# Kernel optimization log

Hardware: AMD Instinct MI355X
Metric: run time of the kernel (lower is better)

## Reference

```python
import jax, jax.numpy as jnp
import numpy as np
import math

N_HEAD = 16
HEAD_DIM = 64
N_EMBD = 1024
EPS_RMS = 1e-5
U_L2_EPS = 1e-6

def _get_alibi_slopes(n_heads):
    def pow2(n):
        start = 2 ** (-2 ** (-(math.log2(n) - 3)))
        return [start * start ** i for i in range(n)]
    if math.log2(n_heads).is_integer():
        return pow2(n_heads)
    c = 2 ** math.floor(math.log2(n_heads))
    s = pow2(c)
    extra = _get_alibi_slopes(2 * c)
    return s + extra[0::2][: n_heads - c]

def setup_inputs() -> dict:
    key = jax.random.key(0)
    ks = jax.random.split(key, 9)
    B, T = 2, 2048
    H, D, C = N_HEAD, HEAD_DIM, N_EMBD
    x = jax.random.normal(ks[0], (B, T, C), dtype=jnp.float32)
    # Linear weights stored as [in, out] so y = x @ W
    sc = 1.0 / math.sqrt(C)
    Wq = jax.random.normal(ks[1], (C, H * D), dtype=jnp.float32) * sc
    Wk = jax.random.normal(ks[2], (C, H * D), dtype=jnp.float32) * sc
    Wv = jax.random.normal(ks[3], (C, H * D), dtype=jnp.float32) * sc
    Wproj = jax.random.normal(ks[4], (H * D, C), dtype=jnp.float32) * (0.5 / math.sqrt(C) / math.sqrt(12))
    q_rms_w = jnp.ones((D,), dtype=jnp.float32)
    k_rms_w = jnp.ones((D,), dtype=jnp.float32)
    # keygated bias params: omega init = softplus_inverse(1.0), u ~ N(0, 1/sqrt(D))
    omega = jnp.full((H,), math.log(math.expm1(1.0)), dtype=jnp.float32)
    u = jax.random.normal(ks[5], (H, D), dtype=jnp.float32) * (1.0 / math.sqrt(D))
    return {"x": x, "Wq": Wq, "Wk": Wk, "Wv": Wv, "Wproj": Wproj,
            "q_rms_w": q_rms_w, "k_rms_w": k_rms_w, "omega": omega, "u": u}

def _rmsnorm(x, w):
    var = jnp.mean(jnp.square(x), axis=-1, keepdims=True)
    return x * jax.lax.rsqrt(var + EPS_RMS) * w

def reference(x, Wq, Wk, Wv, Wproj, q_rms_w, k_rms_w, omega, u):
    B, T, C = x.shape
    H, D = N_HEAD, HEAD_DIM
    q = (x @ Wq).reshape(B, T, H, D)
    k = (x @ Wk).reshape(B, T, H, D)
    v = (x @ Wv).reshape(B, T, H, D)
    q = _rmsnorm(q, q_rms_w)
    k = _rmsnorm(k, k_rms_w)
    # key-gated additive bias
    slopes = jnp.asarray(_get_alibi_slopes(H), dtype=jnp.float32)  # [H]
    omega_eff = jax.nn.softplus(omega) * slopes                    # [H]
    u_n = u / jnp.maximum(jnp.linalg.norm(u, axis=-1, keepdims=True), U_L2_EPS)
    gate_logits = jnp.einsum('bthd,hd->bht', k, u_n) / math.sqrt(D)  # fp32
    gate = jax.nn.softplus(gate_logits)                            # [B,H,T]
    idx = jnp.arange(T)
    dist = jnp.maximum(idx[:, None] - idx[None, :], 0).astype(jnp.float32)  # [T,T]
    bias = -dist[None, None] * omega_eff[None, :, None, None] * gate[:, :, None, :]  # [B,H,T,T]
    causal = idx[:, None] >= idx[None, :]
    bias = jnp.where(causal[None, None], bias, -jnp.inf)
    # attention
    scale = 1.0 / math.sqrt(D)
    scores = jnp.einsum('bihd,bjhd->bhij', q, k) * scale + bias
    attn = jax.nn.softmax(scores, axis=-1)
    y = jnp.einsum('bhij,bjhd->bihd', attn, v).reshape(B, T, H * D)
    return y @ Wproj
```

## Files before the change

### kernel.cpp

```cpp
#include <hip/hip_runtime.h>
#include <hip/hip_bf16.h>

#define NH 16
#define HD 64
#define CE 1024
#define TT 2048
#define BB 2
#define MR (BB*TT)
#define SWZ(r) ((((r) & 7)) ^ (((r) >> 3) & 3))

typedef __attribute__((ext_vector_type(4))) float f32x4;
typedef __attribute__((ext_vector_type(16))) float f32x16;
typedef __attribute__((ext_vector_type(8))) short s16x8;
typedef unsigned int u32;
typedef unsigned short u16;

__device__ __forceinline__ void gld16(const void* g, void* l) {
  __builtin_amdgcn_global_load_lds((const __attribute__((address_space(1))) unsigned int*)g,
                                   (__attribute__((address_space(3))) unsigned int*)l, 16, 0, 0);
}
__device__ __forceinline__ u16 f2b(float f) {
  union { __hip_bfloat16 b; u16 u; } t;
  t.b = __float2bfloat16(f);
  return t.u;
}
__device__ __forceinline__ u32 pk2(float a, float b) {
  return (u32)f2b(a) | ((u32)f2b(b) << 16);
}
__device__ __forceinline__ float red64_sum(float v) {
#pragma unroll
  for (int m = 1; m < 64; m <<= 1) v += __shfl_xor(v, m, 64);
  return v;
}
__device__ __forceinline__ float softplusf(float x) {
  return x > 20.0f ? x : log1pf(expf(x));
}

__global__ __launch_bounds__(256) void cvt_x(const float* __restrict__ x,
                                             u16* __restrict__ xb, int n4) {
  int stride = gridDim.x * blockDim.x;
  for (int i = blockIdx.x * blockDim.x + threadIdx.x; i < n4; i += stride) {
    float4 v = ((const float4*)x)[i];
    union { u16 u[4]; uint2 p; } o;
    o.u[0] = f2b(v.x); o.u[1] = f2b(v.y); o.u[2] = f2b(v.z); o.u[3] = f2b(v.w);
    ((uint2*)xb)[i] = o.p;
  }
}

__global__ __launch_bounds__(256) void cvt_wt(const float* __restrict__ W0, const float* __restrict__ W1,
                                              const float* __restrict__ W2, const float* __restrict__ W3,
                                              u16* __restrict__ T0, u16* __restrict__ T1,
                                              u16* __restrict__ T2, u16* __restrict__ T3) {
  const float* W = blockIdx.z == 0 ? W0 : blockIdx.z == 1 ? W1 : blockIdx.z == 2 ? W2 : W3;
  u16* T = blockIdx.z == 0 ? T0 : blockIdx.z == 1 ? T1 : blockIdx.z == 2 ? T2 : T3;
  __shared__ float t[64][65];
  int k0 = blockIdx.x * 64, n0 = blockIdx.y * 64;
  int row = threadIdx.x >> 2, seg = threadIdx.x & 3;
#pragma unroll
  for (int i = 0; i < 4; ++i) {
    float4 v = *(const float4*)(W + (size_t)(k0 + row) * CE + n0 + seg * 16 + i * 4);
    int c = seg * 16 + i * 4;
    t[row][c + 0] = v.x; t[row][c + 1] = v.y; t[row][c + 2] = v.z; t[row][c + 3] = v.w;
  }
  __syncthreads();
#pragma unroll
  for (int it = 0; it < 2; ++it) {
    int c = threadIdx.x + it * 256;
    int n = c >> 3, ks = (c & 7) * 8;
    union { u16 u[8]; uint4 p; } o;
#pragma unroll
    for (int e = 0; e < 8; ++e) o.u[e] = f2b(t[ks + e][n]);
    *(uint4*)(T + (size_t)(n0 + n) * CE + k0 + ks) = o.p;
  }
}

#define BM 128
#define BN 128
#define BK 64
__global__ __launch_bounds__(256) void gemm3(const u16* __restrict__ A,
    const u16* __restrict__ B0, const u16* __restrict__ B1,
    const u16* __restrict__ B2,
    float* __restrict__ C0, float* __restrict__ C1, float* __restrict__ C2,
    int M, int N, int K) {
  const u16* Bt = blockIdx.z == 0 ? B0 : blockIdx.z == 1 ? B1 : B2;
  float* C = blockIdx.z == 0 ? C0 : blockIdx.z == 1 ? C1 : C2;
  __shared__ __align__(16) u16 aT[BM * BK];
  __shared__ __align__(16) u16 bT[BN * BK];
  int tid = threadIdx.x;
  int w = tid >> 6, lane = tid & 63, q4 = lane >> 4, r16 = lane & 15;
  int m0 = blockIdx.y * BM, n0 = blockIdx.x * BN;
  int wm = (w >> 1) * 64, wn = (w & 1) * 64;
  f32x4 acc[4][4] = {};
  for (int k0 = 0; k0 < K; k0 += BK) {
#pragma unroll
    for (int it = 0; it < 4; ++it) {
      int c = tid + it * 256;
      int row = c >> 3, sl = c & 7;
      gld16(A + (size_t)(m0 + row) * K + k0 + ((sl ^ SWZ(row)) << 3), &aT[c * 8]);
      gld16(Bt + (size_t)(n0 + row) * K + k0 + ((sl ^ SWZ(row)) << 3), &bT[c * 8]);
    }
    __syncthreads();
#pragma unroll
    for (int kk = 0; kk < 2; ++kk) {
      s16x8 af[4], bfr[4];
#pragma unroll
      for (int i = 0; i < 4; ++i) {
        int ra = wm + i * 16 + r16;
        af[i] = *(const s16x8*)((char*)aT + ra * 128 + ((((kk << 2) | q4) ^ SWZ(ra)) << 4));
        int rb = wn + i * 16 + r16;
        bfr[i] = *(const s16x8*)((char*)bT + rb * 128 + ((((kk << 2) | q4) ^ SWZ(rb)) << 4));
      }
#pragma unroll
      for (int i = 0; i < 4; ++i)
#pragma unroll
        for (int j = 0; j < 4; ++j)
          acc[i][j] = __builtin_amdgcn_mfma_f32_16x16x32_bf16(af[i], bfr[j], acc[i][j], 0, 0, 0);
    }
    __syncthreads();
  }
#pragma unroll
  for (int i = 0; i < 4; ++i)
#pragma unroll
    for (int j = 0; j < 4; ++j)
#pragma unroll
      for (int r = 0; r < 4; ++r) {
        int gm = m0 + wm + i * 16 + (q4 << 2) + r;
        int gn = n0 + wn + j * 16 + r16;
        C[(size_t)gm * N + gn] = acc[i][j][r];
      }
}

__global__ __launch_bounds__(256) void rmsgate(const float* __restrict__ q, const float* __restrict__ k,
    const float* __restrict__ v, const float* __restrict__ qw, const float* __restrict__ kw,
    const float* __restrict__ omega, const float* __restrict__ u,
    u16* __restrict__ qb, u16* __restrict__ kb,
    u16* __restrict__ vtb, float* __restrict__ cg) {
  int b = blockIdx.z, h = blockIdx.y, t0 = blockIdx.x * 64;
  int tid = threadIdx.x, w = tid >> 6, lane = tid & 63;
  float uv = u[h * HD + lane];
  float us = red64_sum(uv * uv);
  float un = uv / fmaxf(sqrtf(us), 1e-6f);
  float qwl = qw[lane], kwl = kw[lane];
  float weff = softplusf(omega[h]) * exp2f(-0.5f * (float)(h + 1));
  size_t hb = ((size_t)(b * NH + h)) * TT;
#pragma unroll 4
  for (int it = 0; it < 16; ++it) {
    int t = t0 + w * 16 + it;
    size_t roff = ((size_t)(b * TT + t)) * CE + h * HD + lane;
    float qv = q[roff];
    float rq = rsqrtf(red64_sum(qv * qv) * (1.0f / 64.0f) + 1e-5f);
    qb[(hb + t) * HD + lane] = f2b(qv * rq * qwl * 0.125f);
    float kv = k[roff];
    float rk = rsqrtf(red64_sum(kv * kv) * (1.0f / 64.0f) + 1e-5f);
    float kn = kv * rk * kwl;
    kb[(hb + t) * HD + lane] = f2b(kn);
    float gl = red64_sum(kn * un) * 0.125f;
    if (lane == 0) cg[hb + t] = weff * softplusf(gl);
  }
  __shared__ u16 vt[64 * 65];
  int row = tid >> 2, seg = tid & 3;
#pragma unroll
  for (int i = 0; i < 4; ++i) {
    float4 vv = *(const float4*)(v + ((size_t)(b * TT + t0 + row)) * CE + h * HD + seg * 16 + i * 4);
    int d = seg * 16 + i * 4;
    vt[(d + 0) * 65 + row] = f2b(vv.x);
    vt[(d + 1) * 65 + row] = f2b(vv.y);
    vt[(d + 2) * 65 + row] = f2b(vv.z);
    vt[(d + 3) * 65 + row] = f2b(vv.w);
  }
  __syncthreads();
#pragma unroll
  for (int it = 0; it < 2; ++it) {
    int c = tid + it * 256;
    int d = c >> 3, js = (c & 7) * 8;
    union { u16 u[8]; uint4 p; } o;
#pragma unroll
    for (int e = 0; e < 8; ++e) o.u[e] = vt[d * 65 + js + e];
    *(uint4*)(vtb + (((size_t)(b * NH + h)) * HD + d) * TT + t0 + js) = o.p;
  }
}

#define KVB 64
__global__ __launch_bounds__(256) void attn(const u16* __restrict__ qb,
    const u16* __restrict__ kb, const u16* __restrict__ vtb,
    const float* __restrict__ cg, u16* __restrict__ y) {
  int b = blockIdx.z, h = blockIdx.y, qb0 = blockIdx.x * 128;
  int tid = threadIdx.x, w = tid >> 6, lane = tid & 63;
  int hi = lane >> 5, q5 = lane & 31;
  __shared__ __align__(16) u16 kl[64 * 64];
  __shared__ __align__(16) u16 vl[64 * 64];
  __shared__ float cgl[KVB];
  size_t hb = ((size_t)(b * NH + h)) * TT;
  size_t vbase = ((size_t)(b * NH + h)) * HD;
  int qrow = qb0 + w * 32 + q5;
  s16x8 qf[4];
#pragma unroll
  for (int kc = 0; kc < 4; ++kc)
    qf[kc] = *(const s16x8*)(qb + (hb + qrow) * HD + kc * 16 + hi * 8);
  f32x16 accO[2] = {};
  float m = -1e30f, l = 0.f;
  int qhi = qb0 + w * 32 + 31;
  int nt = (qb0 + 128) / KVB;
  for (int jt = 0; jt < nt; ++jt) {
    int j0 = jt * KVB;
#pragma unroll
    for (int it = 0; it < 2; ++it) {
      int c = tid + (it << 8);
      int row = c >> 3, sl = c & 7;
      gld16(kb + (hb + j0 + row) * HD + ((sl ^ SWZ(row)) << 3), &kl[c * 8]);
      gld16(vtb + (vbase + row) * TT + j0 + ((sl ^ SWZ(row)) << 3), &vl[c * 8]);
    }
    if (tid < KVB) cgl[tid] = cg[hb + j0 + tid];
    __syncthreads();
    if (j0 <= qhi) {
      f32x16 s0 = {}, s1 = {};
#pragma unroll
      for (int kc = 0; kc < 4; ++kc) {
        int r0 = q5;
        s16x8 kf0 = *(const s16x8*)((char*)kl + r0 * 128 + ((((kc << 1) | hi) ^ SWZ(r0)) << 4));
        s0 = __builtin_amdgcn_mfma_f32_32x32x16_bf16(kf0, qf[kc], s0, 0, 0, 0);
        int r1 = q5 + 32;
        s16x8 kf1 = *(const s16x8*)((char*)kl + r1 * 128 + ((((kc << 1) | hi) ^ SWZ(r1)) << 4));
        s1 = __builtin_amdgcn_mfma_f32_32x32x16_bf16(kf1, qf[kc], s1, 0, 0, 0);
      }
      float pmax = -1e30f;
#pragma unroll
      for (int r = 0; r < 16; ++r) {
        int kvl = (r & 3) + 8 * (r >> 2) + 4 * hi;
        int j = j0 + kvl;
        float sv = s0[r];
        sv = (j <= qrow) ? sv - (float)(qrow - j) * cgl[kvl] : -1e30f;
        s0[r] = sv; pmax = fmaxf(pmax, sv);
        int j2 = j0 + 32 + kvl;
        float sv1 = s1[r];
        sv1 = (j2 <= qrow) ? sv1 - (float)(qrow - j2) * cgl[32 + kvl] : -1e30f;
        s1[r] = sv1; pmax = fmaxf(pmax, sv1);
      }
      pmax = fmaxf(pmax, __shfl_xor(pmax, 32, 64));
      float mn = fmaxf(m, pmax);
      float al = __expf(m - mn);
      m = mn;
      float ps = 0.f;
#pragma unroll
      for (int r = 0; r < 16; ++r) {
        float p0 = __expf(s0[r] - m); s0[r] = p0;
        float p1 = __expf(s1[r] - m); s1[r] = p1;
        ps += p0 + p1;
      }
      ps += __shfl_xor(ps, 32, 64);
      l = l * al + ps;
#pragma unroll
      for (int r = 0; r < 16; ++r) { accO[0][r] *= al; accO[1][r] *= al; }
      auto pvchunk = [&](f32x16 sc, int cb4) {
        u32 c01 = pk2(sc[0], sc[1]),  c23 = pk2(sc[2], sc[3]);
        u32 c45 = pk2(sc[4], sc[5]),  c67 = pk2(sc[6], sc[7]);
        u32 c89 = pk2(sc[8], sc[9]),  cAB = pk2(sc[10], sc[11]);
        u32 cCD = pk2(sc[12], sc[13]), cEF = pk2(sc[14], sc[15]);
        u32 x01 = (u32)__shfl_xor((int)c01, 32, 64), x23 = (u32)__shfl_xor((int)c23, 32, 64);
        u32 x45 = (u32)__shfl_xor((int)c45, 32, 64), x67 = (u32)__shfl_xor((int)c67, 32, 64);
        u32 x89 = (u32)__shfl_xor((int)c89, 32, 64), xAB = (u32)__shfl_xor((int)cAB, 32, 64);
        u32 xCD = (u32)__shfl_xor((int)cCD, 32, 64), xEF = (u32)__shfl_xor((int)cEF, 32, 64);
        union { u32 wd[4]; s16x8 v; } Bf0, Bf1;
        Bf0.wd[0] = hi ? x45 : c01; Bf0.wd[1] = hi ? x67 : c23;
        Bf0.wd[2] = hi ? c45 : x01; Bf0.wd[3] = hi ? c67 : x23;
        Bf1.wd[0] = hi ? xCD : c89; Bf1.wd[1] = hi ? xEF : cAB;
        Bf1.wd[2] = hi ? cCD : x89; Bf1.wd[3] = hi ? cEF : xAB;
#pragma unroll
        for (int dt = 0; dt < 2; ++dt) {
          int dr = q5 + 32 * dt;
          s16x8 vf0 = *(const s16x8*)((char*)vl + dr * 128 + (((cb4 | hi) ^ SWZ(dr)) << 4));
          s16x8 vf1 = *(const s16x8*)((char*)vl + dr * 128 + ((((cb4 | 2) | hi) ^ SWZ(dr)) << 4));
          accO[dt] = __builtin_amdgcn_mfma_f32_32x32x16_bf16(vf0, Bf0.v, accO[dt], 0, 0, 0);
          accO[dt] = __builtin_amdgcn_mfma_f32_32x32x16_bf16(vf1, Bf1.v, accO[dt], 0, 0, 0);
        }
      };
      pvchunk(s0, 0);
      pvchunk(s1, 4);
    }
    __syncthreads();
  }
  u16* obase = (w < 2) ? (kl + w * 2048) : (vl + (w - 2) * 2048);
  float inv = 1.f / l;
#pragma unroll
  for (int dt = 0; dt < 2; ++dt)
#pragma unroll
    for (int r = 0; r < 16; ++r) {
      int d = 32 * dt + (r & 3) + 8 * (r >> 2) + 4 * hi;
      *(u16*)((char*)obase + q5 * 128 + ((((d >> 3)) ^ SWZ(q5)) << 4) + ((d & 7) << 1)) = f2b(accO[dt][r] * inv);
    }
  __syncthreads();
  int row = lane >> 1, half = lane & 1;
#pragma unroll
  for (int s4 = 0; s4 < 4; ++s4) {
    int slot = half * 4 + s4;
    s16x8 vv = *(const s16x8*)((char*)obase + row * 128 + ((slot ^ SWZ(row)) << 4));
    *(s16x8*)(y + ((size_t)(b * TT) + qb0 + w * 32 + row) * CE + h * HD + half * 32 + s4 * 8) = vv;
  }
}

extern "C" void kernel_launch(void* const* d_in, const int* in_sizes, int n_in,
                              void* d_out, int out_size, void* d_ws, size_t ws_size,
                              hipStream_t stream) {
  const float* x  = (const float*)d_in[0];
  const float* Wq = (const float*)d_in[1];
  const float* Wk = (const float*)d_in[2];
  const float* Wv = (const float*)d_in[3];
  const float* Wp = (const float*)d_in[4];
  const float* qw = (const float*)d_in[5];
  const float* kw = (const float*)d_in[6];
  const float* om = (const float*)d_in[7];
  const float* u  = (const float*)d_in[8];
  float* out = (float*)d_out;
  char* ws = (char*)d_ws;
  const size_t MB = 1024 * 1024;
  u16* xb  = (u16*)(ws + 0);
  u16* wqt = (u16*)(ws + 8 * MB);
  u16* wkt = (u16*)(ws + 10 * MB);
  u16* wvt = (u16*)(ws + 12 * MB);
  u16* wpt = (u16*)(ws + 14 * MB);
  float* qf = (float*)(ws + 16 * MB);
  float* kf = (float*)(ws + 32 * MB);
  float* vf = (float*)(ws + 48 * MB);
  u16* qbb = (u16*)(ws + 64 * MB);
  u16* kbb = (u16*)(ws + 72 * MB);
  u16* vtb = (u16*)(ws + 80 * MB);
  float* cg = (float*)(ws + 88 * MB);
  u16* yb = (u16*)(ws + 16 * MB);

  cvt_x<<<dim3(2048), dim3(256), 0, stream>>>(x, xb, MR * CE / 4);
  cvt_wt<<<dim3(16, 16, 4), dim3(256), 0, stream>>>(Wq, Wk, Wv, Wp, wqt, wkt, wvt, wpt);
  gemm3<<<dim3(8, 32, 3), dim3(256), 0, stream>>>(xb, wqt, wkt, wvt, qf, kf, vf, MR, CE, CE);
  rmsgate<<<dim3(32, 16, 2), dim3(256), 0, stream>>>(qf, kf, vf, qw, kw, om, u, qbb, kbb, vtb, cg);
  attn<<<dim3(16, 16, 2), dim3(256), 0, stream>>>(qbb, kbb, vtb, cg, yb);
  gemm3<<<dim3(8, 32, 1), dim3(256), 0, stream>>>(yb, wpt, wpt, wpt, out, out, out, MR, CE, CE);
}
```

Before: 307.3 us.

## Restructure attention into single-wave blocks loading K/V straight to registers

Result: slower. 325.7 us (+6.0%).

```diff
diff --git a/kernel.cpp b/kernel.cpp
--- a/kernel.cpp
+++ b/kernel.cpp
@@ -8,6 +8,7 @@
 #define BB 2
 #define MR (BB*TT)
 #define SWZ(r) ((((r) & 7)) ^ (((r) >> 3) & 3))
+#define LOG2E 1.44269504f
 
 typedef __attribute__((ext_vector_type(4))) float f32x4;
 typedef __attribute__((ext_vector_type(16))) float f32x16;
@@ -141,7 +142,7 @@
   float us = red64_sum(uv * uv);
   float un = uv / fmaxf(sqrtf(us), 1e-6f);
   float qwl = qw[lane], kwl = kw[lane];
-  float weff = softplusf(omega[h]) * exp2f(-0.5f * (float)(h + 1));
+  float weff = softplusf(omega[h]) * exp2f(-0.5f * (float)(h + 1)) * LOG2E;
   size_t hb = ((size_t)(b * NH + h)) * TT;
 #pragma unroll 4
   for (int it = 0; it < 16; ++it) {
@@ -149,7 +150,7 @@
     size_t roff = ((size_t)(b * TT + t)) * CE + h * HD + lane;
     float qv = q[roff];
     float rq = rsqrtf(red64_sum(qv * qv) * (1.0f / 64.0f) + 1e-5f);
-    qb[(hb + t) * HD + lane] = f2b(qv * rq * qwl * 0.125f);
+    qb[(hb + t) * HD + lane] = f2b(qv * rq * qwl * (0.125f * LOG2E));
     float kv = k[roff];
     float rk = rsqrtf(red64_sum(kv * kv) * (1.0f / 64.0f) + 1e-5f);
     float kn = kv * rk * kwl;
@@ -181,120 +182,131 @@
 }
 
 #define KVB 64
-__global__ __launch_bounds__(256) void attn(const u16* __restrict__ qb,
+__global__ __launch_bounds__(64) void attn(const u16* __restrict__ qb,
     const u16* __restrict__ kb, const u16* __restrict__ vtb,
     const float* __restrict__ cg, u16* __restrict__ y) {
-  int b = blockIdx.z, h = blockIdx.y, qb0 = blockIdx.x * 128;
-  int tid = threadIdx.x, w = tid >> 6, lane = tid & 63;
+  int b = blockIdx.z, h = blockIdx.y;
+  int qt = gridDim.x - 1 - blockIdx.x;
+  int lane = threadIdx.x & 63;
   int hi = lane >> 5, q5 = lane & 31;
-  __shared__ __align__(16) u16 kl[64 * 64];
-  __shared__ __align__(16) u16 vl[64 * 64];
-  __shared__ float cgl[KVB];
+  __shared__ __align__(16) u16 ol[32 * 64];
   size_t hb = ((size_t)(b * NH + h)) * TT;
   size_t vbase = ((size_t)(b * NH + h)) * HD;
-  int qrow = qb0 + w * 32 + q5;
+  int qrow = qt * 32 + q5;
+  const u16* qptr = qb + (hb + qrow) * HD;
   s16x8 qf[4];
 #pragma unroll
   for (int kc = 0; kc < 4; ++kc)
-    qf[kc] = *(const s16x8*)(qb + (hb + qrow) * HD + kc * 16 + hi * 8);
+    qf[kc] = *(const s16x8*)(qptr + kc * 16 + hi * 8);
   f32x16 accO[2] = {};
   float m = -1e30f, l = 0.f;
-  int qhi = qb0 + w * 32 + 31;
-  int nt = (qb0 + 128) / KVB;
+  int nt = qt / 2 + 1;
   for (int jt = 0; jt < nt; ++jt) {
     int j0 = jt * KVB;
-#pragma unroll
-    for (int it = 0; it < 2; ++it) {
-      int c = tid + (it << 8);
-      int row = c >> 3, sl = c & 7;
-      gld16(kb + (hb + j0 + row) * HD + ((sl ^ SWZ(row)) << 3), &kl[c * 8]);
-      gld16(vtb + (vbase + row) * TT + j0 + ((sl ^ SWZ(row)) << 3), &vl[c * 8]);
-    }
-    if (tid < KVB) cgl[tid] = cg[hb + j0 + tid];
-    __syncthreads();
-    if (j0 <= qhi) {
-      f32x16 s0 = {}, s1 = {};
-#pragma unroll
-      for (int kc = 0; kc < 4; ++kc) {
-        int r0 = q5;
-        s16x8 kf0 = *(const s16x8*)((char*)kl + r0 * 128 + ((((kc << 1) | hi) ^ SWZ(r0)) << 4));
-        s0 = __builtin_amdgcn_mfma_f32_32x32x16_bf16(kf0, qf[kc], s0, 0, 0, 0);
-        int r1 = q5 + 32;
-        s16x8 kf1 = *(const s16x8*)((char*)kl + r1 * 128 + ((((kc << 1) | hi) ^ SWZ(r1)) << 4));
-        s1 = __builtin_amdgcn_mfma_f32_32x32x16_bf16(kf1, qf[kc], s1, 0, 0, 0);
-      }
-      float pmax = -1e30f;
-#pragma unroll
-      for (int r = 0; r < 16; ++r) {
-        int kvl = (r & 3) + 8 * (r >> 2) + 4 * hi;
-        int j = j0 + kvl;
-        float sv = s0[r];
-        sv = (j <= qrow) ? sv - (float)(qrow - j) * cgl[kvl] : -1e30f;
-        s0[r] = sv; pmax = fmaxf(pmax, sv);
-        int j2 = j0 + 32 + kvl;
-        float sv1 = s1[r];
-        sv1 = (j2 <= qrow) ? sv1 - (float)(qrow - j2) * cgl[32 + kvl] : -1e30f;
-        s1[r] = sv1; pmax = fmaxf(pmax, sv1);
-      }
-      pmax = fmaxf(pmax, __shfl_xor(pmax, 32, 64));
-      float mn = fmaxf(m, pmax);
-      float al = __expf(m - mn);
-      m = mn;
-      float ps = 0.f;
-#pragma unroll
-      for (int r = 0; r < 16; ++r) {
-        float p0 = __expf(s0[r] - m); s0[r] = p0;
-        float p1 = __expf(s1[r] - m); s1[r] = p1;
-        ps += p0 + p1;
-      }
-      ps += __shfl_xor(ps, 32, 64);
-      l = l * al + ps;
-#pragma unroll
-      for (int r = 0; r < 16; ++r) { accO[0][r] *= al; accO[1][r] *= al; }
-      auto pvchunk = [&](f32x16 sc, int cb4) {
-        u32 c01 = pk2(sc[0], sc[1]),  c23 = pk2(sc[2], sc[3]);
-        u32 c45 = pk2(sc[4], sc[5]),  c67 = pk2(sc[6], sc[7]);
-        u32 c89 = pk2(sc[8], sc[9]),  cAB = pk2(sc[10], sc[11]);
-        u32 cCD = pk2(sc[12], sc[13]), cEF = pk2(sc[14], sc[15]);
-        u32 x01 = (u32)__shfl_xor((int)c01, 32, 64), x23 = (u32)__shfl_xor((int)c23, 32, 64);
-        u32 x45 = (u32)__shfl_xor((int)c45, 32, 64), x67 = (u32)__shfl_xor((int)c67, 32, 64);
-        u32 x89 = (u32)__shfl_xor((int)c89, 32, 64), xAB = (u32)__shfl_xor((int)cAB, 32, 64);
-        u32 xCD = (u32)__shfl_xor((int)cCD, 32, 64), xEF = (u32)__shfl_xor((int)cEF, 32, 64);
-        union { u32 wd[4]; s16x8 v; } Bf0, Bf1;
-        Bf0.wd[0] = hi ? x45 : c01; Bf0.wd[1] = hi ? x67 : c23;
-        Bf0.wd[2] = hi ? c45 : x01; Bf0.wd[3] = hi ? c67 : x23;
-        Bf1.wd[0] = hi ? xCD : c89; Bf1.wd[1] = hi ? xEF : cAB;
-        Bf1.wd[2] = hi ? cCD : x89; Bf1.wd[3] = hi ? cEF : xAB;
-#pragma unroll
-        for (int dt = 0; dt < 2; ++dt) {
-          int dr = q5 + 32 * dt;
-          s16x8 vf0 = *(const s16x8*)((char*)vl + dr * 128 + (((cb4 | hi) ^ SWZ(dr)) << 4));
-          s16x8 vf1 = *(const s16x8*)((char*)vl + dr * 128 + ((((cb4 | 2) | hi) ^ SWZ(dr)) << 4));
-          accO[dt] = __builtin_amdgcn_mfma_f32_32x32x16_bf16(vf0, Bf0.v, accO[dt], 0, 0, 0);
-          accO[dt] = __builtin_amdgcn_mfma_f32_32x32x16_bf16(vf1, Bf1.v, accO[dt], 0, 0, 0);
-        }
-      };
-      pvchunk(s0, 0);
-      pvchunk(s1, 4);
-    }
-    __syncthreads();
-  }
-  u16* obase = (w < 2) ? (kl + w * 2048) : (vl + (w - 2) * 2048);
+    const u16* kp0 = kb + (hb + j0 + q5) * HD + hi * 8;
+    const u16* kp1 = kb + (hb + j0 + 32 + q5) * HD + hi * 8;
+    s16x8 kf0[4], kf1[4];
+#pragma unroll
+    for (int kc = 0; kc < 4; ++kc) {
+      kf0[kc] = *(const s16x8*)(kp0 + kc * 16);
+      kf1[kc] = *(const s16x8*)(kp1 + kc * 16);
+    }
+    const u16* vp0 = vtb + (vbase + q5) * TT + j0 + hi * 8;
+    const u16* vp1 = vtb + (vbase + 32 + q5) * TT + j0 + hi * 8;
+    s16x8 vfr0[4], vfr1[4];
+#pragma unroll
+    for (int c = 0; c < 4; ++c) {
+      vfr0[c] = *(const s16x8*)(vp0 + c * 16);
+      vfr1[c] = *(const s16x8*)(vp1 + c * 16);
+    }
+    const float* cgp = cg + hb + j0 + 4 * hi;
+    f32x4 cgA[4], cgB[4];
+#pragma unroll
+    for (int g = 0; g < 4; ++g) {
+      cgA[g] = *(const f32x4*)(cgp + 8 * g);
+      cgB[g] = *(const f32x4*)(cgp + 32 + 8 * g);
+    }
+    f32x16 s0 = {}, s1 = {};
+#pragma unroll
+    for (int kc = 0; kc < 4; ++kc) {
+      s0 = __builtin_amdgcn_mfma_f32_32x32x16_bf16(kf0[kc], qf[kc], s0, 0, 0, 0);
+      s1 = __builtin_amdgcn_mfma_f32_32x32x16_bf16(kf1[kc], qf[kc], s1, 0, 0, 0);
+    }
+    float dif0 = (float)(qrow - j0);
+#pragma unroll
+    for (int r = 0; r < 16; ++r) {
+      float kvlf = (float)((r & 3) + 8 * (r >> 2) + 4 * hi);
+      float d0 = dif0 - kvlf;
+      float d1 = d0 - 32.f;
+      float cg0 = cgA[r >> 2][r & 3], cg1 = cgB[r >> 2][r & 3];
+      s0[r] = (d0 >= 0.f) ? s0[r] - d0 * cg0 : -1e30f;
+      s1[r] = (d1 >= 0.f) ? s1[r] - d1 * cg1 : -1e30f;
+    }
+    float t8[8];
+#pragma unroll
+    for (int i = 0; i < 8; ++i)
+      t8[i] = fmaxf(fmaxf(s0[i], s0[i + 8]), fmaxf(s1[i], s1[i + 8]));
+    float t4a = fmaxf(t8[0], t8[4]), t4b = fmaxf(t8[1], t8[5]);
+    float t4c = fmaxf(t8[2], t8[6]), t4d = fmaxf(t8[3], t8[7]);
+    float pmax = fmaxf(fmaxf(t4a, t4b), fmaxf(t4c, t4d));
+    pmax = fmaxf(pmax, __shfl_xor(pmax, 32, 64));
+    float mn = fmaxf(m, pmax);
+    float al = exp2f(m - mn);
+    m = mn;
+#pragma unroll
+    for (int r = 0; r < 16; ++r) {
+      s0[r] = exp2f(s0[r] - m);
+      s1[r] = exp2f(s1[r] - m);
+    }
+    float e8[8];
+#pragma unroll
+    for (int i = 0; i < 8; ++i)
+      e8[i] = (s0[i] + s0[i + 8]) + (s1[i] + s1[i + 8]);
+    float e4a = e8[0] + e8[4], e4b = e8[1] + e8[5];
+    float e4c = e8[2] + e8[6], e4d = e8[3] + e8[7];
+    float ps = (e4a + e4b) + (e4c + e4d);
+    ps += __shfl_xor(ps, 32, 64);
+    l = l * al + ps;
+#pragma unroll
+    for (int r = 0; r < 16; ++r) { accO[0][r] *= al; accO[1][r] *= al; }
+    auto pvchunk = [&](const f32x16& sc, const s16x8& v00, const s16x8& v01,
+                       const s16x8& v10, const s16x8& v11) {
+      u32 c01 = pk2(sc[0], sc[1]),  c23 = pk2(sc[2], sc[3]);
+      u32 c45 = pk2(sc[4], sc[5]),  c67 = pk2(sc[6], sc[7]);
+      u32 c89 = pk2(sc[8], sc[9]),  cAB = pk2(sc[10], sc[11]);
+      u32 cCD = pk2(sc[12], sc[13]), cEF = pk2(sc[14], sc[15]);
+      u32 x01 = (u32)__shfl_xor((int)c01, 32, 64), x23 = (u32)__shfl_xor((int)c23, 32, 64);
+      u32 x45 = (u32)__shfl_xor((int)c45, 32, 64), x67 = (u32)__shfl_xor((int)c67, 32, 64);
+      u32 x89 = (u32)__shfl_xor((int)c89, 32, 64), xAB = (u32)__shfl_xor((int)cAB, 32, 64);
+      u32 xCD = (u32)__shfl_xor((int)cCD, 32, 64), xEF = (u32)__shfl_xor((int)cEF, 32, 64);
+      union { u32 wd[4]; s16x8 v; } Bf0, Bf1;
+      Bf0.wd[0] = hi ? x45 : c01; Bf0.wd[1] = hi ? x67 : c23;
+      Bf0.wd[2] = hi ? c45 : x01; Bf0.wd[3] = hi ? c67 : x23;
+      Bf1.wd[0] = hi ? xCD : c89; Bf1.wd[1] = hi ? xEF : cAB;
+      Bf1.wd[2] = hi ? cCD : x89; Bf1.wd[3] = hi ? cEF : xAB;
+      accO[0] = __builtin_amdgcn_mfma_f32_32x32x16_bf16(v00, Bf0.v, accO[0], 0, 0, 0);
+      accO[0] = __builtin_amdgcn_mfma_f32_32x32x16_bf16(v01, Bf1.v, accO[0], 0, 0, 0);
+      accO[1] = __builtin_amdgcn_mfma_f32_32x32x16_bf16(v10, Bf0.v, accO[1], 0, 0, 0);
+      accO[1] = __builtin_amdgcn_mfma_f32_32x32x16_bf16(v11, Bf1.v, accO[1], 0, 0, 0);
+    };
+    pvchunk(s0, vfr0[0], vfr0[1], vfr1[0], vfr1[1]);
+    pvchunk(s1, vfr0[2], vfr0[3], vfr1[2], vfr1[3]);
+  }
   float inv = 1.f / l;
 #pragma unroll
   for (int dt = 0; dt < 2; ++dt)
 #pragma unroll
     for (int r = 0; r < 16; ++r) {
       int d = 32 * dt + (r & 3) + 8 * (r >> 2) + 4 * hi;
-      *(u16*)((char*)obase + q5 * 128 + ((((d >> 3)) ^ SWZ(q5)) << 4) + ((d & 7) << 1)) = f2b(accO[dt][r] * inv);
+      *(u16*)((char*)ol + q5 * 128 + (((d >> 3) ^ SWZ(q5)) << 4) + ((d & 7) << 1)) = f2b(accO[dt][r] * inv);
     }
   __syncthreads();
   int row = lane >> 1, half = lane & 1;
 #pragma unroll
   for (int s4 = 0; s4 < 4; ++s4) {
     int slot = half * 4 + s4;
-    s16x8 vv = *(const s16x8*)((char*)obase + row * 128 + ((slot ^ SWZ(row)) << 4));
-    *(s16x8*)(y + ((size_t)(b * TT) + qb0 + w * 32 + row) * CE + h * HD + half * 32 + s4 * 8) = vv;
+    s16x8 vv = *(const s16x8*)((char*)ol + row * 128 + ((slot ^ SWZ(row)) << 4));
+    *(s16x8*)(y + ((size_t)(b * TT) + qt * 32 + row) * CE + h * HD + half * 32 + s4 * 8) = vv;
   }
 }
 
@@ -331,6 +343,6 @@
   cvt_wt<<<dim3(16, 16, 4), dim3(256), 0, stream>>>(Wq, Wk, Wv, Wp, wqt, wkt, wvt, wpt);
   gemm3<<<dim3(8, 32, 3), dim3(256), 0, stream>>>(xb, wqt, wkt, wvt, qf, kf, vf, MR, CE, CE);
   rmsgate<<<dim3(32, 16, 2), dim3(256), 0, stream>>>(qf, kf, vf, qw, kw, om, u, qbb, kbb, vtb, cg);
-  attn<<<dim3(16, 16, 2), dim3(256), 0, stream>>>(qbb, kbb, vtb, cg, yb);
+  attn<<<dim3(64, 16, 2), dim3(64), 0, stream>>>(qbb, kbb, vtb, cg, yb);
   gemm3<<<dim3(8, 32, 1), dim3(256), 0, stream>>>(yb, wpt, wpt, wpt, out, out, out, MR, CE, CE);
 }
```
